# Performance work log

Hardware: AMD Instinct MI355X
Metric: run time of the kernel (lower is better)

The kernel has to match this reference:

```python
import jax, jax.numpy as jnp
import numpy as np

N_NODES = 100000
N_EDGES = 1600000
IN_DIM, HID_DIM, OUT_DIM = 128, 64, 1


def setup_inputs() -> dict:
    key = jax.random.key(0)
    ks = jax.random.split(key, 8)
    x = jax.random.normal(ks[0], (N_NODES, IN_DIM), dtype=jnp.float32)
    edge_index = jax.random.randint(ks[1], (2, N_EDGES), 0, N_NODES, dtype=jnp.int64)
    # Glorot-ish scaled weights
    W1 = jax.random.normal(ks[2], (IN_DIM, HID_DIM), dtype=jnp.float32) / np.sqrt(IN_DIM)
    b1 = jnp.zeros((HID_DIM,), dtype=jnp.float32)
    W2 = jax.random.normal(ks[3], (HID_DIM, HID_DIM), dtype=jnp.float32) / np.sqrt(HID_DIM)
    b2 = jnp.zeros((HID_DIM,), dtype=jnp.float32)
    W3 = jax.random.normal(ks[4], (HID_DIM, OUT_DIM), dtype=jnp.float32) / np.sqrt(HID_DIM)
    b3 = jnp.zeros((OUT_DIM,), dtype=jnp.float32)
    return {"x": x, "edge_index": edge_index, "W1": W1, "b1": b1,
            "W2": W2, "b2": b2, "W3": W3, "b3": b3}


def _gcn_norm(edge_index, num_nodes):
    # PyG gcn_norm with add_self_loops=True, edge_weight=1:
    # deg[i] = 1 (self loop) + #incoming edges at i (dst = edge_index[1])
    dst = edge_index[1]
    deg = jnp.ones((num_nodes,), dtype=jnp.float32).at[dst].add(1.0)
    dis = jnp.where(deg > 0, 1.0 / jnp.sqrt(deg), 0.0)  # deg_inv_sqrt
    return dis


def _gcn_conv(x, W, b, src, dst, dis):
    h = x @ W                                   # [N, F_out] transform first (PyG order)
    norm = dis[src] * dis[dst]                  # [E]
    msg = h[src] * norm[:, None]                # gather + scale, [E, F_out]
    out = jnp.zeros_like(h).at[dst].add(msg)    # scatter-add aggregation
    out = out + h * (dis * dis)[:, None]        # self-loop contribution
    return out + b


def reference(x, edge_index, W1, b1, W2, b2, W3, b3):
    src, dst = edge_index[0], edge_index[1]
    dis = _gcn_norm(edge_index, x.shape[0])
    h = jax.nn.relu(_gcn_conv(x, W1, b1, src, dst, dis))   # dropout = identity (eval)
    h = jax.nn.relu(_gcn_conv(h, W2, b2, src, dst, dis))
    return _gcn_conv(h, W3, b3, src, dst, dis)
```

## Files before the change

### kernel.cpp

```cpp
#include <hip/hip_runtime.h>

#define IN_DIM 128
#define HID 64
#define MAXC 400
#define MAXB 256
#define EPB 8192
#define DPT 1024

static __device__ __forceinline__ unsigned short f2bf(float f) {
    unsigned u = __float_as_uint(f);
    u += 0x7FFF + ((u >> 16) & 1);
    return (unsigned short)(u >> 16);
}

typedef short bf16x8 __attribute__((ext_vector_type(8)));
typedef float f32x4 __attribute__((ext_vector_type(4)));

__global__ __launch_bounds__(256) void k_hist2(const int* __restrict__ dst,
                                               int* __restrict__ hmat, int E, int NC) {
    __shared__ int h[MAXC];
    int tid = threadIdx.x, blk = blockIdx.x;
    for (int i = tid; i < NC; i += 256) h[i] = 0;
    __syncthreads();
    int e0 = blk * EPB, e1 = min(e0 + EPB, E);
    for (int e = e0 + tid; e < e1; e += 256) atomicAdd(&h[dst[e] >> 8], 1);
    __syncthreads();
    for (int i = tid; i < NC; i += 256) hmat[blk * MAXC + i] = h[i];
}

__global__ __launch_bounds__(256) void k_bktscan(int* __restrict__ hmat,
                                                 int* __restrict__ bktTotal,
                                                 int NBLK, int NC) {
    __shared__ int tmp[256];
    int cb = blockIdx.x;
    int t = threadIdx.x;
    int v = (t < NBLK) ? hmat[t * MAXC + cb] : 0;
    tmp[t] = v;
    __syncthreads();
    for (int off = 1; off < 256; off <<= 1) {
        int a = (t >= off) ? tmp[t - off] : 0;
        __syncthreads();
        tmp[t] += a;
        __syncthreads();
    }
    if (t < NBLK) hmat[t * MAXC + cb] = tmp[t] - v;
    if (t == 255) bktTotal[cb] = tmp[255];
}

__global__ __launch_bounds__(512) void k_cscan(const int* __restrict__ bktTotal,
                                               int* __restrict__ coarseStart,
                                               int* __restrict__ rowStart,
                                               int NC, int N, int E) {
    __shared__ int tmp[512];
    int t = threadIdx.x;
    int v = (t < NC) ? bktTotal[t] : 0;
    tmp[t] = v;
    __syncthreads();
    for (int off = 1; off < 512; off <<= 1) {
        int a = (t >= off) ? tmp[t - off] : 0;
        __syncthreads();
        tmp[t] += a;
        __syncthreads();
    }
    int excl = tmp[t] - v;
    if (t < NC) coarseStart[t] = excl;
    if (t == NC - 1) coarseStart[NC] = excl + v;
    if (t == 0) rowStart[N] = E;
}

__global__ __launch_bounds__(256) void k_part1(const int* __restrict__ src,
                                               const int* __restrict__ dst,
                                               const int* __restrict__ hmat,
                                               const int* __restrict__ coarseStart,
                                               int* __restrict__ tmp1,
                                               int E, int NC) {
    __shared__ int bcnt[MAXC];
    __shared__ int bbase[MAXC];
    int tid = threadIdx.x, blk = blockIdx.x;
    for (int i = tid; i < NC; i += 256) {
        bcnt[i] = 0;
        bbase[i] = coarseStart[i] + hmat[blk * MAXC + i];
    }
    __syncthreads();
    int e0 = blk * EPB, e1 = min(e0 + EPB, E);
    for (int e = e0 + tid; e < e1; e += 256) {
        int s = src[e], d = dst[e];
        int cb = d >> 8;
        int slot = bbase[cb] + atomicAdd(&bcnt[cb], 1);
        tmp1[slot] = s | ((d & 255) << 17);
    }
}

__global__ __launch_bounds__(DPT) void k_degplace(const int* __restrict__ tmp1,
                                                  const int* __restrict__ coarseStart,
                                                  float* __restrict__ dis,
                                                  int* __restrict__ rowStart,
                                                  int* __restrict__ esrc, int N) {
    __shared__ int hist[256];
    __shared__ int scn[256];
    __shared__ int cur[256];
    int tid = threadIdx.x;
    int cb = blockIdx.x;
    int node0 = cb << 8;
    const int r0 = coarseStart[cb], r1 = coarseStart[cb + 1];
    if (tid < 256) hist[tid] = 0;
    __syncthreads();
    for (int i = r0 + tid; i < r1; i += DPT)
        atomicAdd(&hist[((unsigned)tmp1[i]) >> 17], 1);
    __syncthreads();
    int v = 0;
    if (tid < 256) { v = hist[tid]; scn[tid] = v; }
    __syncthreads();
    for (int off = 1; off < 256; off <<= 1) {
        int a = 0;
        if (tid < 256 && tid >= off) a = scn[tid - off];
        __syncthreads();
        if (tid < 256) scn[tid] += a;
        __syncthreads();
    }
    if (tid < 256) {
        int myStart = r0 + scn[tid] - v;
        cur[tid] = myStart;
        int node = node0 + tid;
        if (node < N) {
            dis[node] = rsqrtf((float)v + 1.0f);
            rowStart[node] = myStart;
        }
    }
    __syncthreads();
    for (int i = r0 + tid; i < r1; i += DPT) {
        int pk = tmp1[i];
        int dl = ((unsigned)pk) >> 17;
        int pos = atomicAdd(&cur[dl], 1);
        esrc[pos] = (pk & 0x1FFFF) << 7;
    }
}

template <int K, typename T>
__global__ __launch_bounds__(256) void k_mmx(const T* __restrict__ X,
                                             const float* __restrict__ W,
                                             const float* __restrict__ dis,
                                             unsigned short* __restrict__ Hbs, int N) {
    constexpr int WP = K + 8;
    __shared__ unsigned short Wt[64 * WP];
    const int tid = threadIdx.x;
    for (int i = tid; i < K * 64; i += 256) {
        int k = i >> 6, n = i & 63;
        Wt[n * WP + k] = f2bf(W[i]);
    }
    __syncthreads();
    const int lane = tid & 63;
    const int m16 = lane & 15;
    const int quad = lane >> 4;
    const int rowBase = blockIdx.x * 64 + (tid >> 6) * 16;
    const int rowc = min(rowBase + m16, N - 1);

    f32x4 acc0 = {0.f, 0.f, 0.f, 0.f};
    f32x4 acc1 = acc0, acc2 = acc0, acc3 = acc0;
    const T* xrow = X + (size_t)rowc * K;
#pragma unroll
    for (int k0 = 0; k0 < K; k0 += 32) {
        bf16x8 af;
        if constexpr (sizeof(T) == 4) {
            const float* xp = (const float*)xrow + k0 + quad * 8;
            float4 xa = *(const float4*)xp;
            float4 xb = *(const float4*)(xp + 4);
            af[0] = (short)f2bf(xa.x); af[1] = (short)f2bf(xa.y);
            af[2] = (short)f2bf(xa.z); af[3] = (short)f2bf(xa.w);
            af[4] = (short)f2bf(xb.x); af[5] = (short)f2bf(xb.y);
            af[6] = (short)f2bf(xb.z); af[7] = (short)f2bf(xb.w);
        } else {
            af = *(const bf16x8*)((const unsigned short*)xrow + k0 + quad * 8);
        }
        const unsigned short* wp = &Wt[m16 * WP + k0 + quad * 8];
        bf16x8 b0 = *(const bf16x8*)(wp);
        bf16x8 b1 = *(const bf16x8*)(wp + 16 * WP);
        bf16x8 b2 = *(const bf16x8*)(wp + 32 * WP);
        bf16x8 b3 = *(const bf16x8*)(wp + 48 * WP);
        acc0 = __builtin_amdgcn_mfma_f32_16x16x32_bf16(af, b0, acc0, 0, 0, 0);
        acc1 = __builtin_amdgcn_mfma_f32_16x16x32_bf16(af, b1, acc1, 0, 0, 0);
        acc2 = __builtin_amdgcn_mfma_f32_16x16x32_bf16(af, b2, acc2, 0, 0, 0);
        acc3 = __builtin_amdgcn_mfma_f32_16x16x32_bf16(af, b3, acc3, 0, 0, 0);
    }
#pragma unroll
    for (int reg = 0; reg < 4; ++reg) {
        int r = rowBase + quad * 4 + reg;
        if (r < N) {
            float dsc = dis[r];
            unsigned short* hp = Hbs + (size_t)r * 64 + m16;
            hp[0]  = f2bf(acc0[reg] * dsc);
            hp[16] = f2bf(acc1[reg] * dsc);
            hp[32] = f2bf(acc2[reg] * dsc);
            hp[48] = f2bf(acc3[reg] * dsc);
        }
    }
}

#define GNODE2(ACC, RA, RB)                                                    \
    {                                                                          \
        int j0 = max(RA - base, 0);                                            \
        int j1 = min(RB - base, cnt);                                          \
        int j = j0;                                                            \
        for (; j + 4 <= j1; j += 4) {                                          \
            unsigned o1 = __shfl(eoff, j + g, 64);                             \
            unsigned o2 = __shfl(eoff, j + 2 + g, 64);                         \
            unsigned d1 = *(const unsigned*)(hbase + o1);                      \
            unsigned d2 = *(const unsigned*)(hbase + o2);                      \
            ACC.x += __uint_as_float(d1 << 16);                                \
            ACC.y += __uint_as_float(d1 & 0xFFFF0000u);                        \
            ACC.x += __uint_as_float(d2 << 16);                                \
            ACC.y += __uint_as_float(d2 & 0xFFFF0000u);                        \
        }                                                                      \
        for (; j < j1; j += 2) {                                               \
            int idx = j + g;                                                   \
            bool valid = idx < j1;                                             \
            unsigned o = __shfl(eoff, valid ? idx : j0, 64);                   \
            unsigned d = *(const unsigned*)(hbase + o);                        \
            d = valid ? d : 0u;                                                \
            ACC.x += __uint_as_float(d << 16);                                 \
            ACC.y += __uint_as_float(d & 0xFFFF0000u);                         \
        }                                                                      \
    }

template <int MODE>
__global__ __launch_bounds__(256) void k_gather64(const unsigned short* __restrict__ Hbs,
                                                  const int* __restrict__ esrc,
                                                  const int* __restrict__ rowStart,
                                                  const float* __restrict__ dis,
                                                  const float* __restrict__ b,
                                                  unsigned short* __restrict__ outB,
                                                  const float* __restrict__ W3,
                                                  const float* __restrict__ b3,
                                                  float* __restrict__ colS,
                                                  float* __restrict__ outF,
                                                  int N) {
    int lane = threadIdx.x & 63;
    int l = lane & 31;
    int g = lane >> 5;
    int wave = (blockIdx.x * 256 + threadIdx.x) >> 6;
    int g0 = wave * 4;
    if (g0 >= N) return;
    const char* hbase = (const char*)Hbs + l * 4;

    int rb = rowStart[min(g0 + lane, N)];
    int R0 = __shfl(rb, 0, 64), R1 = __shfl(rb, 1, 64);
    int R2 = __shfl(rb, 2, 64), R3 = __shfl(rb, 3, 64);
    int R4 = __shfl(rb, 4, 64);
    float dv = dis[min(g0 + lane, N - 1)];
    float d0 = __shfl(dv, 0, 64), d1 = __shfl(dv, 1, 64);
    float d2 = __shfl(dv, 2, 64), d3 = __shfl(dv, 3, 64);
    float2 bl = ((const float2*)b)[l];

    float2 a0 = {0.f, 0.f}, a1 = {0.f, 0.f}, a2 = {0.f, 0.f}, a3 = {0.f, 0.f};
    {
        int n0 = (g == 0) ? g0 : min(g0 + 2, N - 1);
        int n1 = (g == 0) ? min(g0 + 1, N - 1) : min(g0 + 3, N - 1);
        unsigned s0 = *(const unsigned*)(hbase + (size_t)n0 * 128);
        unsigned s1 = *(const unsigned*)(hbase + (size_t)n1 * 128);
        float2 f0 = {__uint_as_float(s0 << 16), __uint_as_float(s0 & 0xFFFF0000u)};
        float2 f1 = {__uint_as_float(s1 << 16), __uint_as_float(s1 & 0xFFFF0000u)};
        if (g == 0) { a0 = f0; a1 = f1; } else { a2 = f0; a3 = f1; }
    }

    for (int base = R0; base < R4; base += 64) {
        int cnt = min(64, R4 - base);
        unsigned eoff = (lane < cnt) ? (unsigned)esrc[base + lane] : 0u;
        GNODE2(a0, R0, R1)
        GNODE2(a1, R1, R2)
        GNODE2(a2, R2, R3)
        GNODE2(a3, R3, R4)
    }

    a0.x += __shfl_xor(a0.x, 32, 64); a0.y += __shfl_xor(a0.y, 32, 64);
    a1.x += __shfl_xor(a1.x, 32, 64); a1.y += __shfl_xor(a1.y, 32, 64);
    a2.x += __shfl_xor(a2.x, 32, 64); a2.y += __shfl_xor(a2.y, 32, 64);
    a3.x += __shfl_xor(a3.x, 32, 64); a3.y += __shfl_xor(a3.y, 32, 64);

    float2 v0 = {fmaxf(a0.x * d0 + bl.x, 0.f), fmaxf(a0.y * d0 + bl.y, 0.f)};
    float2 v1 = {fmaxf(a1.x * d1 + bl.x, 0.f), fmaxf(a1.y * d1 + bl.y, 0.f)};
    float2 v2 = {fmaxf(a2.x * d2 + bl.x, 0.f), fmaxf(a2.y * d2 + bl.y, 0.f)};
    float2 v3 = {fmaxf(a3.x * d3 + bl.x, 0.f), fmaxf(a3.y * d3 + bl.y, 0.f)};

    if (MODE == 1) {
        unsigned p0 = (unsigned)f2bf(v0.x) | ((unsigned)f2bf(v0.y) << 16);
        unsigned p1 = (unsigned)f2bf(v1.x) | ((unsigned)f2bf(v1.y) << 16);
        unsigned p2 = (unsigned)f2bf(v2.x) | ((unsigned)f2bf(v2.y) << 16);
        unsigned p3 = (unsigned)f2bf(v3.x) | ((unsigned)f2bf(v3.y) << 16);
        unsigned* ob = (unsigned*)outB;
        if (g == 0) {
            ob[(size_t)g0 * 32 + l] = p0;
            if (g0 + 1 < N) ob[(size_t)(g0 + 1) * 32 + l] = p1;
        } else {
            if (g0 + 2 < N) ob[(size_t)(g0 + 2) * 32 + l] = p2;
            if (g0 + 3 < N) ob[(size_t)(g0 + 3) * 32 + l] = p3;
        }
    } else {
        float2 w3 = ((const float2*)W3)[l];
        float t0 = v0.x * w3.x + v0.y * w3.y;
        float t1 = v1.x * w3.x + v1.y * w3.y;
        float t2 = v2.x * w3.x + v2.y * w3.y;
        float t3 = v3.x * w3.x + v3.y * w3.y;
#pragma unroll
        for (int off = 1; off <= 16; off <<= 1) {
            t0 += __shfl_xor(t0, off, 64);
            t1 += __shfl_xor(t1, off, 64);
            t2 += __shfl_xor(t2, off, 64);
            t3 += __shfl_xor(t3, off, 64);
        }
        if (lane == 0) {
            float bb = b3[0];
            colS[g0] = t0 * d0;
            outF[g0] = t0 * d0 * d0 + bb;
            if (g0 + 1 < N) { colS[g0 + 1] = t1 * d1; outF[g0 + 1] = t1 * d1 * d1 + bb; }
            if (g0 + 2 < N) { colS[g0 + 2] = t2 * d2; outF[g0 + 2] = t2 * d2 * d2 + bb; }
            if (g0 + 3 < N) { colS[g0 + 3] = t3 * d3; outF[g0 + 3] = t3 * d3 * d3 + bb; }
        }
    }
}

__global__ __launch_bounds__(256) void k_gather1(const float* __restrict__ colS,
                                                 const int* __restrict__ esrc,
                                                 const int* __restrict__ rowStart,
                                                 const float* __restrict__ dis,
                                                 float* __restrict__ out, int N) {
    int i = blockIdx.x * 256 + threadIdx.x;
    if (i >= N) return;
    int r0 = rowStart[i], r1 = rowStart[i + 1];
    float acc = 0.0f;
    for (int e = r0; e < r1; ++e) acc += colS[((unsigned)esrc[e]) >> 7];
    out[i] += acc * dis[i];
}

extern "C" void kernel_launch(void* const* d_in, const int* in_sizes, int n_in,
                              void* d_out, int out_size, void* d_ws, size_t ws_size,
                              hipStream_t stream) {
    const float* x  = (const float*)d_in[0];
    const int*   ei = (const int*)d_in[1];
    const float* W1 = (const float*)d_in[2];
    const float* b1 = (const float*)d_in[3];
    const float* W2 = (const float*)d_in[4];
    const float* b2 = (const float*)d_in[5];
    const float* W3 = (const float*)d_in[6];
    const float* b3 = (const float*)d_in[7];
    float* out = (float*)d_out;

    const int N = in_sizes[0] / IN_DIM;
    const int E = in_sizes[1] / 2;
    const int* src = ei;
    const int* dst = ei + E;
    const int NC = (N + 255) >> 8;
    const int NBLK = (E + EPB - 1) / EPB;

    char* w = (char*)d_ws;
    auto alloc = [&](size_t bytes) {
        char* p = w;
        w += (bytes + 1023) & ~(size_t)1023;
        return p;
    };
    float*          dis        = (float*)alloc((size_t)N * 4);
    unsigned short* Hbs        = (unsigned short*)alloc((size_t)N * 64 * 2);
    unsigned short* Hb1        = (unsigned short*)alloc((size_t)N * 64 * 2);
    float*          colS       = (float*)alloc((size_t)N * 4);
    int*            rowStart   = (int*)alloc((size_t)(N + 1) * 4);
    int*            bktTotal   = (int*)alloc((size_t)MAXC * 4);
    int*            coarseStart= (int*)alloc((size_t)(MAXC + 1) * 4);
    int*            hmat       = (int*)alloc((size_t)MAXB * MAXC * 4);
    int*            esrc       = (int*)alloc((size_t)E * 4);
    int*            tmp1       = (int*)alloc((size_t)E * 4);

    const int NB_N  = (N + 255) / 256;
    const int NB_MX = (N + 63) / 64;
    const int NB_G4 = ((N + 3) / 4 * 64 + 255) / 256;

    k_hist2<<<NBLK, 256, 0, stream>>>(dst, hmat, E, NC);
    k_bktscan<<<NC, 256, 0, stream>>>(hmat, bktTotal, NBLK, NC);
    k_cscan<<<1, 512, 0, stream>>>(bktTotal, coarseStart, rowStart, NC, N, E);
    k_part1<<<NBLK, 256, 0, stream>>>(src, dst, hmat, coarseStart, tmp1, E, NC);
    k_degplace<<<NC, DPT, 0, stream>>>(tmp1, coarseStart, dis, rowStart, esrc, N);

    k_mmx<IN_DIM, float><<<NB_MX, 256, 0, stream>>>(x, W1, dis, Hbs, N);
    k_gather64<1><<<NB_G4, 256, 0, stream>>>(Hbs, esrc, rowStart, dis, b1,
                                             Hb1, nullptr, nullptr, nullptr, nullptr, N);

    k_mmx<HID, unsigned short><<<NB_MX, 256, 0, stream>>>(Hb1, W2, dis, Hbs, N);
    k_gather64<2><<<NB_G4, 256, 0, stream>>>(Hbs, esrc, rowStart, dis, b2,
                                             nullptr, W3, b3, colS, out, N);

    k_gather1<<<NB_N, 256, 0, stream>>>(colS, esrc, rowStart, dis, out, N);
}
```

Measured before the change: 261.1 us.

## Widen gather to 8-byte loads across four edge lanes; stage final gather in LDS

The 64-wide bf16 gather kernel now has each lane load 8 bytes (4 features) instead of 4 bytes. Four 16-lane subgroups handle different edges, with 16-edge unrolled steps and a cross-subgroup shuffle reduction. Each subgroup then finalises one node, which simplifies the epilogue. The scalar final-layer gather now loads the block's edge values cooperatively in a coalesced way into LDS before per-node summation, falling back when a block has too many edges. The aim is fewer memory instructions and better coalescing, at the cost of extra shuffles and LDS use.

```diff
diff --git a/kernel.cpp b/kernel.cpp
--- a/kernel.cpp
+++ b/kernel.cpp
@@ -6,6 +6,7 @@
 #define MAXB 256
 #define EPB 8192
 #define DPT 1024
+#define G1CAP 6144
 
 static __device__ __forceinline__ unsigned short f2bf(float f) {
     unsigned u = __float_as_uint(f);
@@ -196,30 +197,61 @@
     }
 }
 
-#define GNODE2(ACC, RA, RB)                                                    \
+
+#define ACCADD(A, D)                                                           \
+    {                                                                          \
+        A.x += __uint_as_float((D).x << 16);                                   \
+        A.y += __uint_as_float((D).x & 0xFFFF0000u);                           \
+        A.z += __uint_as_float((D).y << 16);                                   \
+        A.w += __uint_as_float((D).y & 0xFFFF0000u);                           \
+    }
+
+#define GNODE4(ACC, RA, RB)                                                    \
     {                                                                          \
         int j0 = max(RA - base, 0);                                            \
         int j1 = min(RB - base, cnt);                                          \
         int j = j0;                                                            \
-        for (; j + 4 <= j1; j += 4) {                                          \
-            unsigned o1 = __shfl(eoff, j + g, 64);                             \
-            unsigned o2 = __shfl(eoff, j + 2 + g, 64);                         \
-            unsigned d1 = *(const unsigned*)(hbase + o1);                      \
-            unsigned d2 = *(const unsigned*)(hbase + o2);                      \
-            ACC.x += __uint_as_float(d1 << 16);                                \
-            ACC.y += __uint_as_float(d1 & 0xFFFF0000u);                        \
-            ACC.x += __uint_as_float(d2 << 16);                                \
-            ACC.y += __uint_as_float(d2 & 0xFFFF0000u);                        \
+        for (; j + 16 <= j1; j += 16) {                                        \
+            unsigned o0 = __shfl(eoff, j + sub, 64);                           \
+            unsigned o1 = __shfl(eoff, j + 4 + sub, 64);                       \
+            unsigned o2 = __shfl(eoff, j + 8 + sub, 64);                       \
+            unsigned o3 = __shfl(eoff, j + 12 + sub, 64);                      \
+            uint2 q0 = *(const uint2*)(hb + o0);                               \
+            uint2 q1 = *(const uint2*)(hb + o1);                               \
+            uint2 q2 = *(const uint2*)(hb + o2);                               \
+            uint2 q3 = *(const uint2*)(hb + o3);                               \
+            ACCADD(ACC, q0) ACCADD(ACC, q1) ACCADD(ACC, q2) ACCADD(ACC, q3)    \
         }                                                                      \
-        for (; j < j1; j += 2) {                                               \
-            int idx = j + g;                                                   \
-            bool valid = idx < j1;                                             \
-            unsigned o = __shfl(eoff, valid ? idx : j0, 64);                   \
-            unsigned d = *(const unsigned*)(hbase + o);                        \
-            d = valid ? d : 0u;                                                \
-            ACC.x += __uint_as_float(d << 16);                                 \
-            ACC.y += __uint_as_float(d & 0xFFFF0000u);                         \
+        if (j + 8 <= j1) {                                                     \
+            unsigned o0 = __shfl(eoff, j + sub, 64);                           \
+            unsigned o1 = __shfl(eoff, j + 4 + sub, 64);                       \
+            uint2 q0 = *(const uint2*)(hb + o0);                               \
+            uint2 q1 = *(const uint2*)(hb + o1);                               \
+            ACCADD(ACC, q0) ACCADD(ACC, q1)                                    \
+            j += 8;                                                            \
         }                                                                      \
+        if (j + 4 <= j1) {                                                     \
+            unsigned o0 = __shfl(eoff, j + sub, 64);                           \
+            uint2 q0 = *(const uint2*)(hb + o0);                               \
+            ACCADD(ACC, q0)                                                    \
+            j += 4;                                                            \
+        }                                                                      \
+        if (j < j1) {                                                          \
+            int idx = j + sub;                                                 \
+            bool vld = idx < j1;                                               \
+            unsigned o0 = __shfl(eoff, vld ? idx : j0, 64);                    \
+            uint2 q0 = *(const uint2*)(hb + o0);                               \
+            if (!vld) { q0.x = 0u; q0.y = 0u; }                                \
+            ACCADD(ACC, q0)                                                    \
+        }                                                                      \
+    }
+
+#define REDX(A)                                                                \
+    {                                                                          \
+        A.x += __shfl_xor(A.x, 16, 64); A.y += __shfl_xor(A.y, 16, 64);        \
+        A.z += __shfl_xor(A.z, 16, 64); A.w += __shfl_xor(A.w, 16, 64);        \
+        A.x += __shfl_xor(A.x, 32, 64); A.y += __shfl_xor(A.y, 32, 64);        \
+        A.z += __shfl_xor(A.z, 32, 64); A.w += __shfl_xor(A.w, 32, 64);        \
     }
 
 template <int MODE>
@@ -235,85 +267,72 @@
                                                   float* __restrict__ outF,
                                                   int N) {
     int lane = threadIdx.x & 63;
-    int l = lane & 31;
-    int g = lane >> 5;
+    int c = lane & 15;
+    int sub = lane >> 4;
     int wave = (blockIdx.x * 256 + threadIdx.x) >> 6;
     int g0 = wave * 4;
     if (g0 >= N) return;
-    const char* hbase = (const char*)Hbs + l * 4;
+    const char* hb = (const char*)Hbs + c * 8;
 
     int rb = rowStart[min(g0 + lane, N)];
     int R0 = __shfl(rb, 0, 64), R1 = __shfl(rb, 1, 64);
     int R2 = __shfl(rb, 2, 64), R3 = __shfl(rb, 3, 64);
     int R4 = __shfl(rb, 4, 64);
-    float dv = dis[min(g0 + lane, N - 1)];
-    float d0 = __shfl(dv, 0, 64), d1 = __shfl(dv, 1, 64);
-    float d2 = __shfl(dv, 2, 64), d3 = __shfl(dv, 3, 64);
-    float2 bl = ((const float2*)b)[l];
-
-    float2 a0 = {0.f, 0.f}, a1 = {0.f, 0.f}, a2 = {0.f, 0.f}, a3 = {0.f, 0.f};
+
+    float4 a0 = {0.f, 0.f, 0.f, 0.f}, a1 = a0, a2 = a0, a3 = a0;
     {
-        int n0 = (g == 0) ? g0 : min(g0 + 2, N - 1);
-        int n1 = (g == 0) ? min(g0 + 1, N - 1) : min(g0 + 3, N - 1);
-        unsigned s0 = *(const unsigned*)(hbase + (size_t)n0 * 128);
-        unsigned s1 = *(const unsigned*)(hbase + (size_t)n1 * 128);
-        float2 f0 = {__uint_as_float(s0 << 16), __uint_as_float(s0 & 0xFFFF0000u)};
-        float2 f1 = {__uint_as_float(s1 << 16), __uint_as_float(s1 & 0xFFFF0000u)};
-        if (g == 0) { a0 = f0; a1 = f1; } else { a2 = f0; a3 = f1; }
+        int nself = min(g0 + sub, N - 1);
+        uint2 sd = *(const uint2*)(hb + ((size_t)nself << 7));
+        float4 sf;
+        sf.x = __uint_as_float(sd.x << 16);
+        sf.y = __uint_as_float(sd.x & 0xFFFF0000u);
+        sf.z = __uint_as_float(sd.y << 16);
+        sf.w = __uint_as_float(sd.y & 0xFFFF0000u);
+        if (sub == 0) a0 = sf;
+        else if (sub == 1) a1 = sf;
+        else if (sub == 2) a2 = sf;
+        else a3 = sf;
     }
 
     for (int base = R0; base < R4; base += 64) {
         int cnt = min(64, R4 - base);
         unsigned eoff = (lane < cnt) ? (unsigned)esrc[base + lane] : 0u;
-        GNODE2(a0, R0, R1)
-        GNODE2(a1, R1, R2)
-        GNODE2(a2, R2, R3)
-        GNODE2(a3, R3, R4)
-    }
-
-    a0.x += __shfl_xor(a0.x, 32, 64); a0.y += __shfl_xor(a0.y, 32, 64);
-    a1.x += __shfl_xor(a1.x, 32, 64); a1.y += __shfl_xor(a1.y, 32, 64);
-    a2.x += __shfl_xor(a2.x, 32, 64); a2.y += __shfl_xor(a2.y, 32, 64);
-    a3.x += __shfl_xor(a3.x, 32, 64); a3.y += __shfl_xor(a3.y, 32, 64);
-
-    float2 v0 = {fmaxf(a0.x * d0 + bl.x, 0.f), fmaxf(a0.y * d0 + bl.y, 0.f)};
-    float2 v1 = {fmaxf(a1.x * d1 + bl.x, 0.f), fmaxf(a1.y * d1 + bl.y, 0.f)};
-    float2 v2 = {fmaxf(a2.x * d2 + bl.x, 0.f), fmaxf(a2.y * d2 + bl.y, 0.f)};
-    float2 v3 = {fmaxf(a3.x * d3 + bl.x, 0.f), fmaxf(a3.y * d3 + bl.y, 0.f)};
+        GNODE4(a0, R0, R1)
+        GNODE4(a1, R1, R2)
+        GNODE4(a2, R2, R3)
+        GNODE4(a3, R3, R4)
+    }
+
+    REDX(a0) REDX(a1) REDX(a2) REDX(a3)
+
+    float4 a = a0;
+    if (sub == 1) a = a1;
+    if (sub == 2) a = a2;
+    if (sub == 3) a = a3;
+    int node = g0 + sub;
+    float ds = dis[min(node, N - 1)];
+    float4 bl = ((const float4*)b)[c];
+    float4 v;
+    v.x = fmaxf(a.x * ds + bl.x, 0.f);
+    v.y = fmaxf(a.y * ds + bl.y, 0.f);
+    v.z = fmaxf(a.z * ds + bl.z, 0.f);
+    v.w = fmaxf(a.w * ds + bl.w, 0.f);
 
     if (MODE == 1) {
-        unsigned p0 = (unsigned)f2bf(v0.x) | ((unsigned)f2bf(v0.y) << 16);
-        unsigned p1 = (unsigned)f2bf(v1.x) | ((unsigned)f2bf(v1.y) << 16);
-        unsigned p2 = (unsigned)f2bf(v2.x) | ((unsigned)f2bf(v2.y) << 16);
-        unsigned p3 = (unsigned)f2bf(v3.x) | ((unsigned)f2bf(v3.y) << 16);
-        unsigned* ob = (unsigned*)outB;
-        if (g == 0) {
-            ob[(size_t)g0 * 32 + l] = p0;
-            if (g0 + 1 < N) ob[(size_t)(g0 + 1) * 32 + l] = p1;
-        } else {
-            if (g0 + 2 < N) ob[(size_t)(g0 + 2) * 32 + l] = p2;
-            if (g0 + 3 < N) ob[(size_t)(g0 + 3) * 32 + l] = p3;
-        }
+        uint2 pv;
+        pv.x = (unsigned)f2bf(v.x) | ((unsigned)f2bf(v.y) << 16);
+        pv.y = (unsigned)f2bf(v.z) | ((unsigned)f2bf(v.w) << 16);
+        if (node < N) ((uint2*)outB)[(size_t)node * 16 + c] = pv;
     } else {
-        float2 w3 = ((const float2*)W3)[l];
-        float t0 = v0.x * w3.x + v0.y * w3.y;
-        float t1 = v1.x * w3.x + v1.y * w3.y;
-        float t2 = v2.x * w3.x + v2.y * w3.y;
-        float t3 = v3.x * w3.x + v3.y * w3.y;
-#pragma unroll
-        for (int off = 1; off <= 16; off <<= 1) {
-            t0 += __shfl_xor(t0, off, 64);
-            t1 += __shfl_xor(t1, off, 64);
-            t2 += __shfl_xor(t2, off, 64);
-            t3 += __shfl_xor(t3, off, 64);
-        }
-        if (lane == 0) {
-            float bb = b3[0];
-            colS[g0] = t0 * d0;
-            outF[g0] = t0 * d0 * d0 + bb;
-            if (g0 + 1 < N) { colS[g0 + 1] = t1 * d1; outF[g0 + 1] = t1 * d1 * d1 + bb; }
-            if (g0 + 2 < N) { colS[g0 + 2] = t2 * d2; outF[g0 + 2] = t2 * d2 * d2 + bb; }
-            if (g0 + 3 < N) { colS[g0 + 3] = t3 * d3; outF[g0 + 3] = t3 * d3 * d3 + bb; }
+        float4 w3 = ((const float4*)W3)[c];
+        float t = v.x * w3.x + v.y * w3.y + v.z * w3.z + v.w * w3.w;
+        t += __shfl_xor(t, 1, 64);
+        t += __shfl_xor(t, 2, 64);
+        t += __shfl_xor(t, 4, 64);
+        t += __shfl_xor(t, 8, 64);
+        if (c == 0 && node < N) {
+            colS[node] = t * ds;
+            outF[node] = t * ds * ds + b3[0];
         }
     }
 }
@@ -323,12 +342,33 @@
                                                  const int* __restrict__ rowStart,
                                                  const float* __restrict__ dis,
                                                  float* __restrict__ out, int N) {
-    int i = blockIdx.x * 256 + threadIdx.x;
-    if (i >= N) return;
-    int r0 = rowStart[i], r1 = rowStart[i + 1];
-    float acc = 0.0f;
-    for (int e = r0; e < r1; ++e) acc += colS[((unsigned)esrc[e]) >> 7];
-    out[i] += acc * dis[i];
+    __shared__ float ls[G1CAP];
+    int tid = threadIdx.x;
+    int n0 = blockIdx.x * 256;
+    int nEnd = min(n0 + 256, N);
+    int r0 = rowStart[n0];
+    int r1 = rowStart[nEnd];
+    int cnt = r1 - r0;
+    if (cnt <= G1CAP) {
+        for (int i = tid; i < cnt; i += 256)
+            ls[i] = colS[((unsigned)esrc[r0 + i]) >> 7];
+        __syncthreads();
+        int n = n0 + tid;
+        if (n < N) {
+            int a = rowStart[n] - r0, bnd = rowStart[n + 1] - r0;
+            float acc = 0.0f;
+            for (int e = a; e < bnd; ++e) acc += ls[e];
+            out[n] += acc * dis[n];
+        }
+    } else {
+        int n = n0 + tid;
+        if (n < N) {
+            int a = rowStart[n], bnd = rowStart[n + 1];
+            float acc = 0.0f;
+            for (int e = a; e < bnd; ++e) acc += colS[((unsigned)esrc[e]) >> 7];
+            out[n] += acc * dis[n];
+        }
+    }
 }
 
 extern "C" void kernel_launch(void* const* d_in, const int* in_sizes, int n_in,
```

New measurement: 242.3 us. 7.2% less time.
